# Kernel optimization log

Hardware: AMD Instinct MI355X
Metric: run time of the kernel (lower is better)

The kernel has to match this reference:

```python
import jax, jax.numpy as jnp
import numpy as np


def _lstm_scan(x_tbd, Wih, Whh, bih, bhh):
    """Standard LSTM cell (PyTorch i,f,g,o gate order) scanned over time.
    x_tbd: [T,B,D]; returns hidden states [T,B,H]."""
    H = Whh.shape[1]
    B = x_tbd.shape[1]

    def step(carry, x_t):
        h, c = carry
        gates = x_t @ Wih.T + bih + h @ Whh.T + bhh  # [B,4H]
        i, f, g, o = jnp.split(gates, 4, axis=-1)
        c = jax.nn.sigmoid(f) * c + jax.nn.sigmoid(i) * jnp.tanh(g)
        h = jax.nn.sigmoid(o) * jnp.tanh(c)
        return (h, c), h

    h0 = jnp.zeros((B, H), x_tbd.dtype)
    _, hs = jax.lax.scan(step, (h0, h0), x_tbd)
    return hs


def setup_inputs() -> dict:
    key = jax.random.key(0)
    B, T, D, H = 64, 1024, 512, 256  # output_dim=1024 -> H = output_dim//4 per direction
    ks = jax.random.split(key, 9)
    s = 0.05
    mk = lambda k, shape: jax.random.normal(k, shape, jnp.float32) * s
    return {
        "input": mk(ks[0], (B, T, D)),
        "Wih_f": mk(ks[1], (4 * H, D)), "Whh_f": mk(ks[2], (4 * H, H)),
        "bih_f": mk(ks[3], (4 * H,)),   "bhh_f": mk(ks[4], (4 * H,)),
        "Wih_b": mk(ks[5], (4 * H, D)), "Whh_b": mk(ks[6], (4 * H, H)),
        "bih_b": mk(ks[7], (4 * H,)),   "bhh_b": mk(ks[8], (4 * H,)),
    }


def reference(input, Wih_f, Whh_f, bih_f, bhh_f, Wih_b, Whh_b, bih_b, bhh_b):
    # [B,T,D] -> [T,B,D] for scan over time
    x_tbd = jnp.transpose(input, (1, 0, 2))
    hf = _lstm_scan(x_tbd, Wih_f, Whh_f, bih_f, bhh_f)            # forward in time
    hb = _lstm_scan(x_tbd[::-1], Wih_b, Whh_b, bih_b, bhh_b)[::-1]  # backward, re-aligned
    # output[t] = cat(outputf[t], outputb[T-1-t]) == cat(hf[t], hb_aligned[t])
    out = jnp.concatenate([hf, hb], axis=-1)  # [T,B,2H]
    return jnp.transpose(out, (1, 0, 2))      # [B,T,2H]
```

## Files before the change

### kernel.cpp

```cpp
#include <hip/hip_runtime.h>
#include <hip/hip_bf16.h>

typedef __attribute__((ext_vector_type(8))) short bf8;
typedef __attribute__((ext_vector_type(4))) float f32x4;
typedef __attribute__((ext_vector_type(2))) unsigned int u32x2;

#define T_SEQ 1024

__device__ __forceinline__ float sigm(float x) { return 1.f / (1.f + __expf(-x)); }
__device__ __forceinline__ float tanh_(float x) { return 2.f / (1.f + __expf(-2.f * x)) - 1.f; }

__device__ __forceinline__ short bf16s(float x) {
    union { __hip_bfloat16 h; short s; } u;
    u.h = __float2bfloat16(x);
    return u.s;
}

__device__ __forceinline__ bf8 pack_bf8(const float4 a, const float4 b) {
    bf8 r;
    r[0] = bf16s(a.x); r[1] = bf16s(a.y); r[2] = bf16s(a.z); r[3] = bf16s(a.w);
    r[4] = bf16s(b.x); r[5] = bf16s(b.y); r[6] = bf16s(b.z); r[7] = bf16s(b.w);
    return r;
}

__device__ __forceinline__ void store_sc1_b64(void* p, unsigned int lo, unsigned int hi) {
    u32x2 v; v[0] = lo; v[1] = hi;
    asm volatile("global_store_dwordx2 %0, %1, off sc1" :: "v"(p), "v"(v) : "memory");
}
__device__ __forceinline__ void store_sc1_b32(void* p, unsigned int v) {
    asm volatile("global_store_dword %0, %1, off sc1" :: "v"(p), "v"(v) : "memory");
}
__device__ __forceinline__ unsigned int load_sc1_b32(const void* p) {
    unsigned int v;
    asm volatile("global_load_dword %0, %1, off sc1\n"
                 "s_waitcnt vmcnt(0)"
                 : "=v"(v) : "v"(p) : "memory");
    return v;
}
__device__ __forceinline__ bf8 load_sc1_b128(const void* p) {
    bf8 v;
    asm volatile("global_load_dwordx4 %0, %1, off sc1" : "=v"(v) : "v"(p) : "memory");
    return v;
}

__global__ __launch_bounds__(256) void init_kernel(unsigned int* __restrict__ p, int n)
{
    const int i = blockIdx.x * 256 + threadIdx.x;
    if (i < n) p[i] = 0u;
}

__global__ __launch_bounds__(256) void xproj_kernel(
    const float* __restrict__ X,
    const float* __restrict__ WihF,
    const float* __restrict__ bihF,
    const float* __restrict__ bhhF,
    const float* __restrict__ WihB,
    const float* __restrict__ bihB,
    const float* __restrict__ bhhB,
    __hip_bfloat16* __restrict__ XpF,
    __hip_bfloat16* __restrict__ XpB)
{
    const int dir = blockIdx.z;
    const float* W  = dir ? WihB : WihF;
    const float* bi = dir ? bihB : bihF;
    const float* bh = dir ? bhhB : bhhF;
    __hip_bfloat16* Xp = dir ? XpB : XpF;

    __shared__ __align__(16) short As[128 * 32];
    __shared__ __align__(16) short Bs[128 * 32];

    const int tid  = threadIdx.x;
    const int lane = tid & 63;
    const int w    = tid >> 6;
    const int quad = lane >> 4;
    const int l16  = lane & 15;
    const int wr   = w >> 1, wc = w & 1;

    const int m0 = blockIdx.x * 128;
    const int n0 = blockIdx.y * 128;

    const int srow = tid >> 2;
    const int scg  = tid & 3;

    f32x4 acc[4][4] = {};

    for (int kk = 0; kk < 512; kk += 32) {
        const float* pa0 = X + (size_t)(m0 + srow)      * 512 + kk + scg * 8;
        const float* pa1 = X + (size_t)(m0 + 64 + srow) * 512 + kk + scg * 8;
        const float* pb0 = W + (size_t)(n0 + srow)      * 512 + kk + scg * 8;
        const float* pb1 = W + (size_t)(n0 + 64 + srow) * 512 + kk + scg * 8;
        bf8 a0 = pack_bf8(*(const float4*)pa0, *(const float4*)(pa0 + 4));
        bf8 a1 = pack_bf8(*(const float4*)pa1, *(const float4*)(pa1 + 4));
        bf8 b0 = pack_bf8(*(const float4*)pb0, *(const float4*)(pb0 + 4));
        bf8 b1 = pack_bf8(*(const float4*)pb1, *(const float4*)(pb1 + 4));
        __syncthreads();
        *(bf8*)&As[(srow)      * 32 + scg * 8] = a0;
        *(bf8*)&As[(64 + srow) * 32 + scg * 8] = a1;
        *(bf8*)&Bs[(srow)      * 32 + scg * 8] = b0;
        *(bf8*)&Bs[(64 + srow) * 32 + scg * 8] = b1;
        __syncthreads();

        bf8 af[4], bfr[4];
#pragma unroll
        for (int mt = 0; mt < 4; mt++)
            af[mt] = *(const bf8*)&As[(wr * 64 + mt * 16 + l16) * 32 + quad * 8];
#pragma unroll
        for (int nt = 0; nt < 4; nt++)
            bfr[nt] = *(const bf8*)&Bs[(wc * 64 + nt * 16 + l16) * 32 + quad * 8];
#pragma unroll
        for (int mt = 0; mt < 4; mt++)
#pragma unroll
            for (int nt = 0; nt < 4; nt++)
                acc[mt][nt] = __builtin_amdgcn_mfma_f32_16x16x32_bf16(af[mt], bfr[nt], acc[mt][nt], 0, 0, 0);
    }

#pragma unroll
    for (int nt = 0; nt < 4; nt++) {
        const int n = n0 + wc * 64 + nt * 16 + l16;
        const float bias = bi[n] + bh[n];
#pragma unroll
        for (int mt = 0; mt < 4; mt++) {
#pragma unroll
            for (int r = 0; r < 4; r++) {
                const int m = m0 + wr * 64 + mt * 16 + quad * 4 + r;
                const int b = m >> 10, t = m & 1023;
                Xp[((size_t)t * 64 + b) * 1024 + n] = __float2bfloat16(acc[mt][nt][r] + bias);
            }
        }
    }
}

__global__ __launch_bounds__(256, 1) void lstm_rec_kernel(
    const __hip_bfloat16* __restrict__ XpF,
    const __hip_bfloat16* __restrict__ XpB,
    const float* __restrict__ WhhF,
    const float* __restrict__ WhhB,
    __hip_bfloat16* __restrict__ hexch,
    int* __restrict__ flags,
    float* __restrict__ out)
{
    const int wg  = blockIdx.x;
    const int dir = wg >> 4;
    const int s   = wg & 15;
    const int tid  = threadIdx.x;
    const int lane = tid & 63;
    const int w    = tid >> 6;
    const int quad = lane >> 4;
    const int l16  = lane & 15;

    const __hip_bfloat16* Xp = dir ? XpB : XpF;
    const float* Whh         = dir ? WhhB : WhhF;
    unsigned int* hexchU     = (unsigned int*)hexch;

    __shared__ unsigned int hstage[512];

    bf8 Bf[4][8];
#pragma unroll
    for (int g = 0; g < 4; g++)
#pragma unroll
        for (int k = 0; k < 8; k++) {
            const float* p = Whh + (size_t)(g * 256 + s * 16 + l16) * 256 + k * 32 + quad * 8;
            Bf[g][k] = pack_bf8(*(const float4*)p, *(const float4*)(p + 4));
        }

    float c[4] = {0.f, 0.f, 0.f, 0.f};


    for (int tau = 0; tau < T_SEQ; tau++) {
        const int t = dir ? (T_SEQ - 1 - tau) : tau;

        if (tid < 16) {
            int* f = &flags[(dir * 16 + tid) * 32];
            while ((int)load_sc1_b32(f) < tau) { }
        }
        __syncthreads();

        unsigned short xpu[4][4];
#pragma unroll
        for (int g = 0; g < 4; g++)
#pragma unroll
            for (int r = 0; r < 4; r++) {
                const int b = w * 16 + quad * 4 + r;
                xpu[g][r] = __builtin_nontemporal_load(
                    (const unsigned short*)&Xp[((size_t)t * 64 + b) * 1024 + g * 256 + s * 16 + l16]);
            }

        const __hip_bfloat16* hb = hexch + ((size_t)((tau & 1) * 2 + dir) * 16) * 1024;
        bf8 Af[8];
#pragma unroll
        for (int k = 0; k < 8; k++) {
            const int sA = k * 2 + (quad >> 1);
            Af[k] = load_sc1_b128(hb + (size_t)sA * 1024 + (w * 16 + l16) * 16 + (quad & 1) * 8);
        }
        asm volatile("s_waitcnt vmcnt(0)" ::: "memory");
        __builtin_amdgcn_sched_barrier(0);

        f32x4 acc[4];
        const f32x4 zero = {0.f, 0.f, 0.f, 0.f};
#pragma unroll
        for (int g = 0; g < 4; g++) acc[g] = zero;
#pragma unroll
        for (int k = 0; k < 8; k++)
#pragma unroll
            for (int g = 0; g < 4; g++)
                acc[g] = __builtin_amdgcn_mfma_f32_16x16x32_bf16(Af[k], Bf[g][k], acc[g], 0, 0, 0);

        float hv[4];
#pragma unroll
        for (int r = 0; r < 4; r++) {
            union { unsigned int u; float f; } cv0, cv1, cv2, cv3;
            cv0.u = (unsigned int)xpu[0][r] << 16;
            cv1.u = (unsigned int)xpu[1][r] << 16;
            cv2.u = (unsigned int)xpu[2][r] << 16;
            cv3.u = (unsigned int)xpu[3][r] << 16;
            const float ig = sigm(acc[0][r] + cv0.f);
            const float fg = sigm(acc[1][r] + cv1.f);
            const float gg = tanh_(acc[2][r] + cv2.f);
            const float og = sigm(acc[3][r] + cv3.f);
            c[r] = fg * c[r] + ig * gg;
            hv[r] = og * tanh_(c[r]);
            const int b = w * 16 + quad * 4 + r;
            ((__hip_bfloat16*)hstage)[b * 16 + l16] = __float2bfloat16(hv[r]);
        }
        __syncthreads();

        {
            unsigned int* dst = hexchU + ((size_t)(((tau + 1) & 1) * 2 + dir) * 16 + s) * 512;
            store_sc1_b64(&dst[2 * tid], hstage[2 * tid], hstage[2 * tid + 1]);
        }
        asm volatile("s_waitcnt vmcnt(0)" ::: "memory");
        __syncthreads();
        if (tid == 0)
            store_sc1_b32(&flags[(dir * 16 + s) * 32], (unsigned int)(tau + 1));

#pragma unroll
        for (int r = 0; r < 4; r++) {
            const int b = w * 16 + quad * 4 + r;
            __builtin_nontemporal_store(hv[r], &out[((size_t)b * T_SEQ + t) * 512 + dir * 256 + s * 16 + l16]);
        }
    }
}

extern "C" void kernel_launch(void* const* d_in, const int* in_sizes, int n_in,
                              void* d_out, int out_size, void* d_ws, size_t ws_size,
                              hipStream_t stream)
{
    const float* X    = (const float*)d_in[0];
    const float* WihF = (const float*)d_in[1];
    const float* WhhF = (const float*)d_in[2];
    const float* bihF = (const float*)d_in[3];
    const float* bhhF = (const float*)d_in[4];
    const float* WihB = (const float*)d_in[5];
    const float* WhhB = (const float*)d_in[6];
    const float* bihB = (const float*)d_in[7];
    const float* bhhB = (const float*)d_in[8];
    float* out = (float*)d_out;

    char* ws = (char*)d_ws;
    __hip_bfloat16* XpF   = (__hip_bfloat16*)ws;
    __hip_bfloat16* XpB   = (__hip_bfloat16*)(ws + 134217728);
    __hip_bfloat16* hexch = (__hip_bfloat16*)(ws + 268435456);
    int*            flags = (int*)(ws + 268435456 + 131072);

    const int initN = (131072 + 4096) / 4;
    init_kernel<<<(initN + 255) / 256, 256, 0, stream>>>((unsigned int*)(ws + 268435456), initN);

    dim3 g1(512, 8, 2);
    xproj_kernel<<<g1, 256, 0, stream>>>(X, WihF, bihF, bhhF, WihB, bihB, bhhB, XpF, XpB);
    lstm_rec_kernel<<<32, 256, 0, stream>>>(XpF, XpB, WhhF, WhhB, hexch, flags, out);
}
```

Before: 4.364 ms.

## Replace flag-based handoff with step-tagged hidden-state words in recurrent exchange

```diff
diff --git a/kernel.cpp b/kernel.cpp
--- a/kernel.cpp
+++ b/kernel.cpp
@@ -3,7 +3,7 @@
 
 typedef __attribute__((ext_vector_type(8))) short bf8;
 typedef __attribute__((ext_vector_type(4))) float f32x4;
-typedef __attribute__((ext_vector_type(2))) unsigned int u32x2;
+typedef __attribute__((ext_vector_type(4))) unsigned int u32x4;
 
 #define T_SEQ 1024
 
@@ -23,24 +23,17 @@
     return r;
 }
 
-__device__ __forceinline__ void store_sc1_b64(void* p, unsigned int lo, unsigned int hi) {
-    u32x2 v; v[0] = lo; v[1] = hi;
-    asm volatile("global_store_dwordx2 %0, %1, off sc1" :: "v"(p), "v"(v) : "memory");
-}
 __device__ __forceinline__ void store_sc1_b32(void* p, unsigned int v) {
     asm volatile("global_store_dword %0, %1, off sc1" :: "v"(p), "v"(v) : "memory");
 }
-__device__ __forceinline__ unsigned int load_sc1_b32(const void* p) {
-    unsigned int v;
-    asm volatile("global_load_dword %0, %1, off sc1\n"
-                 "s_waitcnt vmcnt(0)"
-                 : "=v"(v) : "v"(p) : "memory");
-    return v;
-}
-__device__ __forceinline__ bf8 load_sc1_b128(const void* p) {
-    bf8 v;
+__device__ __forceinline__ u32x4 load_sc1_x4(const void* p) {
+    u32x4 v;
     asm volatile("global_load_dwordx4 %0, %1, off sc1" : "=v"(v) : "v"(p) : "memory");
     return v;
+}
+
+__device__ __forceinline__ unsigned short ldnt_u16(const __hip_bfloat16* p) {
+    return __builtin_nontemporal_load((const unsigned short*)p);
 }
 
 __global__ __launch_bounds__(256) void init_kernel(unsigned int* __restrict__ p, int n)
@@ -135,8 +128,7 @@
     const __hip_bfloat16* __restrict__ XpB,
     const float* __restrict__ WhhF,
     const float* __restrict__ WhhB,
-    __hip_bfloat16* __restrict__ hexch,
-    int* __restrict__ flags,
+    unsigned int* __restrict__ ex,
     float* __restrict__ out)
 {
     const int wg  = blockIdx.x;
@@ -150,9 +142,6 @@
 
     const __hip_bfloat16* Xp = dir ? XpB : XpF;
     const float* Whh         = dir ? WhhB : WhhF;
-    unsigned int* hexchU     = (unsigned int*)hexch;
-
-    __shared__ unsigned int hstage[512];
 
     bf8 Bf[4][8];
 #pragma unroll
@@ -165,35 +154,55 @@
 
     float c[4] = {0.f, 0.f, 0.f, 0.f};
 
+    const int crow = quad >> 1;
+    const int coff = (w * 16 + l16) * 16 + (quad & 1) * 8;
+    unsigned int* const exdir = ex + (dir << 14);
 
     for (int tau = 0; tau < T_SEQ; tau++) {
         const int t = dir ? (T_SEQ - 1 - tau) : tau;
 
-        if (tid < 16) {
-            int* f = &flags[(dir * 16 + tid) * 32];
-            while ((int)load_sc1_b32(f) < tau) { }
-        }
-        __syncthreads();
-
         unsigned short xpu[4][4];
 #pragma unroll
         for (int g = 0; g < 4; g++)
 #pragma unroll
             for (int r = 0; r < 4; r++) {
                 const int b = w * 16 + quad * 4 + r;
-                xpu[g][r] = __builtin_nontemporal_load(
-                    (const unsigned short*)&Xp[((size_t)t * 64 + b) * 1024 + g * 256 + s * 16 + l16]);
-            }
-
-        const __hip_bfloat16* hb = hexch + ((size_t)((tau & 1) * 2 + dir) * 16) * 1024;
+                xpu[g][r] = ldnt_u16(&Xp[((size_t)t * 64 + b) * 1024 + g * 256 + s * 16 + l16]);
+            }
+
+        const unsigned int tagw = (unsigned int)tau << 16;
+        unsigned int* const exc = exdir + ((tau & 1) << 15);
+        u32x4 dd[16];
+        int rounds = 0;
+        while (true) {
+#pragma unroll
+            for (int k8 = 0; k8 < 8; k8++) {
+                dd[2 * k8]     = load_sc1_x4(exc + (k8 * 2 + crow) * 1024 + coff);
+                dd[2 * k8 + 1] = load_sc1_x4(exc + (k8 * 2 + crow) * 1024 + coff + 4);
+            }
+            asm volatile("s_waitcnt vmcnt(0)" ::: "memory");
+            __builtin_amdgcn_sched_barrier(0);
+            unsigned int diff = 0;
+#pragma unroll
+            for (int i = 0; i < 16; i++) {
+                diff |= (dd[i][0] ^ tagw) & 0xFFFF0000u;
+                diff |= (dd[i][1] ^ tagw) & 0xFFFF0000u;
+                diff |= (dd[i][2] ^ tagw) & 0xFFFF0000u;
+                diff |= (dd[i][3] ^ tagw) & 0xFFFF0000u;
+            }
+            if (__all(diff == 0)) break;
+            if (++rounds >= 1024) break;
+        }
+
         bf8 Af[8];
 #pragma unroll
-        for (int k = 0; k < 8; k++) {
-            const int sA = k * 2 + (quad >> 1);
-            Af[k] = load_sc1_b128(hb + (size_t)sA * 1024 + (w * 16 + l16) * 16 + (quad & 1) * 8);
-        }
-        asm volatile("s_waitcnt vmcnt(0)" ::: "memory");
-        __builtin_amdgcn_sched_barrier(0);
+        for (int k8 = 0; k8 < 8; k8++) {
+#pragma unroll
+            for (int j = 0; j < 4; j++) {
+                Af[k8][j]     = (short)(dd[2 * k8][j]     & 0xFFFFu);
+                Af[k8][4 + j] = (short)(dd[2 * k8 + 1][j] & 0xFFFFu);
+            }
+        }
 
         f32x4 acc[4];
         const f32x4 zero = {0.f, 0.f, 0.f, 0.f};
@@ -205,6 +214,8 @@
             for (int g = 0; g < 4; g++)
                 acc[g] = __builtin_amdgcn_mfma_f32_16x16x32_bf16(Af[k], Bf[g][k], acc[g], 0, 0, 0);
 
+        const unsigned int pubtag = (unsigned int)(tau + 1) << 16;
+        unsigned int* const dst = exdir + (((tau + 1) & 1) << 15) + (s << 10);
         float hv[4];
 #pragma unroll
         for (int r = 0; r < 4; r++) {
@@ -220,18 +231,9 @@
             c[r] = fg * c[r] + ig * gg;
             hv[r] = og * tanh_(c[r]);
             const int b = w * 16 + quad * 4 + r;
-            ((__hip_bfloat16*)hstage)[b * 16 + l16] = __float2bfloat16(hv[r]);
-        }
-        __syncthreads();
-
-        {
-            unsigned int* dst = hexchU + ((size_t)(((tau + 1) & 1) * 2 + dir) * 16 + s) * 512;
-            store_sc1_b64(&dst[2 * tid], hstage[2 * tid], hstage[2 * tid + 1]);
-        }
-        asm volatile("s_waitcnt vmcnt(0)" ::: "memory");
-        __syncthreads();
-        if (tid == 0)
-            store_sc1_b32(&flags[(dir * 16 + s) * 32], (unsigned int)(tau + 1));
+            store_sc1_b32(&dst[b * 16 + l16],
+                          pubtag | (unsigned int)(unsigned short)bf16s(hv[r]));
+        }
 
 #pragma unroll
         for (int r = 0; r < 4; r++) {
@@ -257,15 +259,14 @@
     float* out = (float*)d_out;
 
     char* ws = (char*)d_ws;
-    __hip_bfloat16* XpF   = (__hip_bfloat16*)ws;
-    __hip_bfloat16* XpB   = (__hip_bfloat16*)(ws + 134217728);
-    __hip_bfloat16* hexch = (__hip_bfloat16*)(ws + 268435456);
-    int*            flags = (int*)(ws + 268435456 + 131072);
-
-    const int initN = (131072 + 4096) / 4;
-    init_kernel<<<(initN + 255) / 256, 256, 0, stream>>>((unsigned int*)(ws + 268435456), initN);
+    __hip_bfloat16* XpF = (__hip_bfloat16*)ws;
+    __hip_bfloat16* XpB = (__hip_bfloat16*)(ws + 134217728);
+    unsigned int*   ex  = (unsigned int*)(ws + 268435456);
+
+    const int initN = 65536;
+    init_kernel<<<initN / 256, 256, 0, stream>>>(ex, initN);
 
     dim3 g1(512, 8, 2);
     xproj_kernel<<<g1, 256, 0, stream>>>(X, WihF, bihF, bhhF, WihB, bihB, bhhB, XpF, XpB);
-    lstm_rec_kernel<<<32, 256, 0, stream>>>(XpF, XpB, WhhF, WhhB, hexch, flags, out);
-}
+    lstm_rec_kernel<<<32, 256, 0, stream>>>(XpF, XpB, WhhF, WhhB, ex, out);
+}
```

Result: slower. 5.335 ms (+22.2%).

## Fuse input projection and recurrence into one kernel with chunked producer-consumer overlap

Applied to the files above, without the earlier changes.

```diff
diff --git a/kernel.cpp b/kernel.cpp
--- a/kernel.cpp
+++ b/kernel.cpp
@@ -29,6 +29,10 @@
 }
 __device__ __forceinline__ void store_sc1_b32(void* p, unsigned int v) {
     asm volatile("global_store_dword %0, %1, off sc1" :: "v"(p), "v"(v) : "memory");
+}
+__device__ __forceinline__ void store_sc1_b16(void* p, unsigned short v) {
+    unsigned int vv = v;
+    asm volatile("global_store_short %0, %1, off sc1" :: "v"(p), "v"(vv) : "memory");
 }
 __device__ __forceinline__ unsigned int load_sc1_b32(const void* p) {
     unsigned int v;
@@ -49,7 +53,7 @@
     if (i < n) p[i] = 0u;
 }
 
-__global__ __launch_bounds__(256) void xproj_kernel(
+__global__ __launch_bounds__(256, 1) void fused_kernel(
     const float* __restrict__ X,
     const float* __restrict__ WihF,
     const float* __restrict__ bihF,
@@ -57,187 +61,201 @@
     const float* __restrict__ WihB,
     const float* __restrict__ bihB,
     const float* __restrict__ bhhB,
+    const float* __restrict__ WhhF,
+    const float* __restrict__ WhhB,
     __hip_bfloat16* __restrict__ XpF,
-    __hip_bfloat16* __restrict__ XpB)
+    __hip_bfloat16* __restrict__ XpB,
+    __hip_bfloat16* __restrict__ hexch,
+    int* __restrict__ flags,
+    int* __restrict__ cnt,
+    float* __restrict__ out)
 {
-    const int dir = blockIdx.z;
-    const float* W  = dir ? WihB : WihF;
-    const float* bi = dir ? bihB : bihF;
-    const float* bh = dir ? bhhB : bhhF;
-    __hip_bfloat16* Xp = dir ? XpB : XpF;
-
-    __shared__ __align__(16) short As[128 * 32];
-    __shared__ __align__(16) short Bs[128 * 32];
-
+    __shared__ __align__(16) unsigned char smem[16384];
     const int tid  = threadIdx.x;
     const int lane = tid & 63;
-    const int w    = tid >> 6;
     const int quad = lane >> 4;
     const int l16  = lane & 15;
-    const int wr   = w >> 1, wc = w & 1;
-
-    const int m0 = blockIdx.x * 128;
-    const int n0 = blockIdx.y * 128;
-
-    const int srow = tid >> 2;
-    const int scg  = tid & 3;
-
-    f32x4 acc[4][4] = {};
-
-    for (int kk = 0; kk < 512; kk += 32) {
-        const float* pa0 = X + (size_t)(m0 + srow)      * 512 + kk + scg * 8;
-        const float* pa1 = X + (size_t)(m0 + 64 + srow) * 512 + kk + scg * 8;
-        const float* pb0 = W + (size_t)(n0 + srow)      * 512 + kk + scg * 8;
-        const float* pb1 = W + (size_t)(n0 + 64 + srow) * 512 + kk + scg * 8;
-        bf8 a0 = pack_bf8(*(const float4*)pa0, *(const float4*)(pa0 + 4));
-        bf8 a1 = pack_bf8(*(const float4*)pa1, *(const float4*)(pa1 + 4));
-        bf8 b0 = pack_bf8(*(const float4*)pb0, *(const float4*)(pb0 + 4));
-        bf8 b1 = pack_bf8(*(const float4*)pb1, *(const float4*)(pb1 + 4));
-        __syncthreads();
-        *(bf8*)&As[(srow)      * 32 + scg * 8] = a0;
-        *(bf8*)&As[(64 + srow) * 32 + scg * 8] = a1;
-        *(bf8*)&Bs[(srow)      * 32 + scg * 8] = b0;
-        *(bf8*)&Bs[(64 + srow) * 32 + scg * 8] = b1;
-        __syncthreads();
-
-        bf8 af[4], bfr[4];
-#pragma unroll
-        for (int mt = 0; mt < 4; mt++)
-            af[mt] = *(const bf8*)&As[(wr * 64 + mt * 16 + l16) * 32 + quad * 8];
-#pragma unroll
-        for (int nt = 0; nt < 4; nt++)
-            bfr[nt] = *(const bf8*)&Bs[(wc * 64 + nt * 16 + l16) * 32 + quad * 8];
-#pragma unroll
-        for (int mt = 0; mt < 4; mt++)
-#pragma unroll
-            for (int nt = 0; nt < 4; nt++)
-                acc[mt][nt] = __builtin_amdgcn_mfma_f32_16x16x32_bf16(af[mt], bfr[nt], acc[mt][nt], 0, 0, 0);
-    }
-
-#pragma unroll
-    for (int nt = 0; nt < 4; nt++) {
-        const int n = n0 + wc * 64 + nt * 16 + l16;
-        const float bias = bi[n] + bh[n];
-#pragma unroll
-        for (int mt = 0; mt < 4; mt++) {
+
+    if (blockIdx.x < 32) {
+        const int wg  = blockIdx.x;
+        const int dir = wg >> 4;
+        const int s   = wg & 15;
+        const int w   = tid >> 6;
+
+        const __hip_bfloat16* Xp = dir ? XpB : XpF;
+        const float* Whh         = dir ? WhhB : WhhF;
+        unsigned int* hexchU     = (unsigned int*)hexch;
+        unsigned int* hstage     = (unsigned int*)smem;
+
+        bf8 Bf[4][8];
+#pragma unroll
+        for (int g = 0; g < 4; g++)
+#pragma unroll
+            for (int k = 0; k < 8; k++) {
+                const float* p = Whh + (size_t)(g * 256 + s * 16 + l16) * 256 + k * 32 + quad * 8;
+                Bf[g][k] = pack_bf8(*(const float4*)p, *(const float4*)(p + 4));
+            }
+
+        float c[4] = {0.f, 0.f, 0.f, 0.f};
+
+        for (int tau = 0; tau < T_SEQ; tau++) {
+            const int t = dir ? (T_SEQ - 1 - tau) : tau;
+
+            if ((tau & 127) == 0) {
+                if (tid == 0) {
+                    const int chunk = dir ? (7 - (tau >> 7)) : (tau >> 7);
+                    const int* cp = &cnt[dir * 8 + chunk];
+                    int guard = 0;
+                    while ((int)load_sc1_b32(cp) < 512 && ++guard < (1 << 20)) { }
+                }
+                __syncthreads();
+            }
+
+            if (tid < 16) {
+                int* f = &flags[(dir * 16 + tid) * 32];
+                while ((int)load_sc1_b32(f) < tau) { }
+            }
+            __syncthreads();
+
+            unsigned short xpu[4][4];
+#pragma unroll
+            for (int g = 0; g < 4; g++)
+#pragma unroll
+                for (int r = 0; r < 4; r++) {
+                    const int b = w * 16 + quad * 4 + r;
+                    xpu[g][r] = __builtin_nontemporal_load(
+                        (const unsigned short*)&Xp[((size_t)t * 64 + b) * 1024 + g * 256 + s * 16 + l16]);
+                }
+
+            const __hip_bfloat16* hb = hexch + ((size_t)((tau & 1) * 2 + dir) * 16) * 1024;
+            bf8 Af[8];
+#pragma unroll
+            for (int k = 0; k < 8; k++) {
+                const int sA = k * 2 + (quad >> 1);
+                Af[k] = load_sc1_b128(hb + (size_t)sA * 1024 + (w * 16 + l16) * 16 + (quad & 1) * 8);
+            }
+            asm volatile("s_waitcnt vmcnt(0)" ::: "memory");
+            __builtin_amdgcn_sched_barrier(0);
+
+            f32x4 acc[4];
+            const f32x4 zero = {0.f, 0.f, 0.f, 0.f};
+#pragma unroll
+            for (int g = 0; g < 4; g++) acc[g] = zero;
+#pragma unroll
+            for (int k = 0; k < 8; k++)
+#pragma unroll
+                for (int g = 0; g < 4; g++)
+                    acc[g] = __builtin_amdgcn_mfma_f32_16x16x32_bf16(Af[k], Bf[g][k], acc[g], 0, 0, 0);
+
+            float hv[4];
 #pragma unroll
             for (int r = 0; r < 4; r++) {
-                const int m = m0 + wr * 64 + mt * 16 + quad * 4 + r;
-                const int b = m >> 10, t = m & 1023;
-                Xp[((size_t)t * 64 + b) * 1024 + n] = __float2bfloat16(acc[mt][nt][r] + bias);
-            }
-        }
-    }
-}
-
-__global__ __launch_bounds__(256, 1) void lstm_rec_kernel(
-    const __hip_bfloat16* __restrict__ XpF,
-    const __hip_bfloat16* __restrict__ XpB,
-    const float* __restrict__ WhhF,
-    const float* __restrict__ WhhB,
-    __hip_bfloat16* __restrict__ hexch,
-    int* __restrict__ flags,
-    float* __restrict__ out)
-{
-    const int wg  = blockIdx.x;
-    const int dir = wg >> 4;
-    const int s   = wg & 15;
-    const int tid  = threadIdx.x;
-    const int lane = tid & 63;
-    const int w    = tid >> 6;
-    const int quad = lane >> 4;
-    const int l16  = lane & 15;
-
-    const __hip_bfloat16* Xp = dir ? XpB : XpF;
-    const float* Whh         = dir ? WhhB : WhhF;
-    unsigned int* hexchU     = (unsigned int*)hexch;
-
-    __shared__ unsigned int hstage[512];
-
-    bf8 Bf[4][8];
-#pragma unroll
-    for (int g = 0; g < 4; g++)
-#pragma unroll
-        for (int k = 0; k < 8; k++) {
-            const float* p = Whh + (size_t)(g * 256 + s * 16 + l16) * 256 + k * 32 + quad * 8;
-            Bf[g][k] = pack_bf8(*(const float4*)p, *(const float4*)(p + 4));
-        }
-
-    float c[4] = {0.f, 0.f, 0.f, 0.f};
-
-
-    for (int tau = 0; tau < T_SEQ; tau++) {
-        const int t = dir ? (T_SEQ - 1 - tau) : tau;
-
-        if (tid < 16) {
-            int* f = &flags[(dir * 16 + tid) * 32];
-            while ((int)load_sc1_b32(f) < tau) { }
-        }
-        __syncthreads();
-
-        unsigned short xpu[4][4];
-#pragma unroll
-        for (int g = 0; g < 4; g++)
+                union { unsigned int u; float f; } cv0, cv1, cv2, cv3;
+                cv0.u = (unsigned int)xpu[0][r] << 16;
+                cv1.u = (unsigned int)xpu[1][r] << 16;
+                cv2.u = (unsigned int)xpu[2][r] << 16;
+                cv3.u = (unsigned int)xpu[3][r] << 16;
+                const float ig = sigm(acc[0][r] + cv0.f);
+                const float fg = sigm(acc[1][r] + cv1.f);
+                const float gg = tanh_(acc[2][r] + cv2.f);
+                const float og = sigm(acc[3][r] + cv3.f);
+                c[r] = fg * c[r] + ig * gg;
+                hv[r] = og * tanh_(c[r]);
+                const int b = w * 16 + quad * 4 + r;
+                ((__hip_bfloat16*)hstage)[b * 16 + l16] = __float2bfloat16(hv[r]);
+            }
+            __syncthreads();
+
+            {
+                unsigned int* dst = hexchU + ((size_t)(((tau + 1) & 1) * 2 + dir) * 16 + s) * 512;
+                store_sc1_b64(&dst[2 * tid], hstage[2 * tid], hstage[2 * tid + 1]);
+            }
+            asm volatile("s_waitcnt vmcnt(0)" ::: "memory");
+            __syncthreads();
+            if (tid == 0)
+                store_sc1_b32(&flags[(dir * 16 + s) * 32], (unsigned int)(tau + 1));
+
 #pragma unroll
             for (int r = 0; r < 4; r++) {
                 const int b = w * 16 + quad * 4 + r;
-                xpu[g][r] = __builtin_nontemporal_load(
-                    (const unsigned short*)&Xp[((size_t)t * 64 + b) * 1024 + g * 256 + s * 16 + l16]);
-            }
-
-        const __hip_bfloat16* hb = hexch + ((size_t)((tau & 1) * 2 + dir) * 16) * 1024;
-        bf8 Af[8];
-#pragma unroll
-        for (int k = 0; k < 8; k++) {
-            const int sA = k * 2 + (quad >> 1);
-            Af[k] = load_sc1_b128(hb + (size_t)sA * 1024 + (w * 16 + l16) * 16 + (quad & 1) * 8);
+                __builtin_nontemporal_store(hv[r], &out[((size_t)b * T_SEQ + t) * 512 + dir * 256 + s * 16 + l16]);
+            }
         }
-        asm volatile("s_waitcnt vmcnt(0)" ::: "memory");
-        __builtin_amdgcn_sched_barrier(0);
-
-        f32x4 acc[4];
-        const f32x4 zero = {0.f, 0.f, 0.f, 0.f};
-#pragma unroll
-        for (int g = 0; g < 4; g++) acc[g] = zero;
-#pragma unroll
-        for (int k = 0; k < 8; k++)
-#pragma unroll
-            for (int g = 0; g < 4; g++)
-                acc[g] = __builtin_amdgcn_mfma_f32_16x16x32_bf16(Af[k], Bf[g][k], acc[g], 0, 0, 0);
-
-        float hv[4];
-#pragma unroll
-        for (int r = 0; r < 4; r++) {
-            union { unsigned int u; float f; } cv0, cv1, cv2, cv3;
-            cv0.u = (unsigned int)xpu[0][r] << 16;
-            cv1.u = (unsigned int)xpu[1][r] << 16;
-            cv2.u = (unsigned int)xpu[2][r] << 16;
-            cv3.u = (unsigned int)xpu[3][r] << 16;
-            const float ig = sigm(acc[0][r] + cv0.f);
-            const float fg = sigm(acc[1][r] + cv1.f);
-            const float gg = tanh_(acc[2][r] + cv2.f);
-            const float og = sigm(acc[3][r] + cv3.f);
-            c[r] = fg * c[r] + ig * gg;
-            hv[r] = og * tanh_(c[r]);
-            const int b = w * 16 + quad * 4 + r;
-            ((__hip_bfloat16*)hstage)[b * 16 + l16] = __float2bfloat16(hv[r]);
+    } else {
+        const int xp4 = blockIdx.x - 32;
+        const int st  = xp4 >> 10;
+        const int r1  = xp4 & 1023;
+        const int dir = r1 >> 9;
+        const int r2  = r1 & 511;
+        const int yb  = r2 >> 6;
+        const int bb  = r2 & 63;
+        const int chunk = dir ? (7 - st) : st;
+        const int m0 = bb * 1024 + chunk * 128;
+        const int n0 = yb * 128;
+
+        const float* W  = dir ? WihB : WihF;
+        const float* bi = dir ? bihB : bihF;
+        const float* bh = dir ? bhhB : bhhF;
+        __hip_bfloat16* Xp = dir ? XpB : XpF;
+
+        short* As = (short*)smem;
+        short* Bs = (short*)(smem + 8192);
+
+        const int w2   = tid >> 6;
+        const int wr   = w2 >> 1, wc = w2 & 1;
+        const int srow = tid >> 2;
+        const int scg  = tid & 3;
+
+        f32x4 acc[4][4] = {};
+
+        for (int kk = 0; kk < 512; kk += 32) {
+            const float* pa0 = X + (size_t)(m0 + srow)      * 512 + kk + scg * 8;
+            const float* pa1 = X + (size_t)(m0 + 64 + srow) * 512 + kk + scg * 8;
+            const float* pb0 = W + (size_t)(n0 + srow)      * 512 + kk + scg * 8;
+            const float* pb1 = W + (size_t)(n0 + 64 + srow) * 512 + kk + scg * 8;
+            bf8 a0 = pack_bf8(*(const float4*)pa0, *(const float4*)(pa0 + 4));
+            bf8 a1 = pack_bf8(*(const float4*)pa1, *(const float4*)(pa1 + 4));
+            bf8 b0 = pack_bf8(*(const float4*)pb0, *(const float4*)(pb0 + 4));
+            bf8 b1 = pack_bf8(*(const float4*)pb1, *(const float4*)(pb1 + 4));
+            __syncthreads();
+            *(bf8*)&As[(srow)      * 32 + scg * 8] = a0;
+            *(bf8*)&As[(64 + srow) * 32 + scg * 8] = a1;
+            *(bf8*)&Bs[(srow)      * 32 + scg * 8] = b0;
+            *(bf8*)&Bs[(64 + srow) * 32 + scg * 8] = b1;
+            __syncthreads();
+
+            bf8 af[4], bfr[4];
+#pragma unroll
+            for (int mt = 0; mt < 4; mt++)
+                af[mt] = *(const bf8*)&As[(wr * 64 + mt * 16 + l16) * 32 + quad * 8];
+#pragma unroll
+            for (int nt = 0; nt < 4; nt++)
+                bfr[nt] = *(const bf8*)&Bs[(wc * 64 + nt * 16 + l16) * 32 + quad * 8];
+#pragma unroll
+            for (int mt = 0; mt < 4; mt++)
+#pragma unroll
+                for (int nt = 0; nt < 4; nt++)
+                    acc[mt][nt] = __builtin_amdgcn_mfma_f32_16x16x32_bf16(af[mt], bfr[nt], acc[mt][nt], 0, 0, 0);
         }
-        __syncthreads();
-
-        {
-            unsigned int* dst = hexchU + ((size_t)(((tau + 1) & 1) * 2 + dir) * 16 + s) * 512;
-            store_sc1_b64(&dst[2 * tid], hstage[2 * tid], hstage[2 * tid + 1]);
+
+#pragma unroll
+        for (int nt = 0; nt < 4; nt++) {
+            const int n = n0 + wc * 64 + nt * 16 + l16;
+            const float bias = bi[n] + bh[n];
+#pragma unroll
+            for (int mt = 0; mt < 4; mt++) {
+#pragma unroll
+                for (int r = 0; r < 4; r++) {
+                    const int m = m0 + wr * 64 + mt * 16 + quad * 4 + r;
+                    const int b = m >> 10, t = m & 1023;
+                    store_sc1_b16(&Xp[((size_t)t * 64 + b) * 1024 + n],
+                                  (unsigned short)bf16s(acc[mt][nt][r] + bias));
+                }
+            }
         }
         asm volatile("s_waitcnt vmcnt(0)" ::: "memory");
         __syncthreads();
-        if (tid == 0)
-            store_sc1_b32(&flags[(dir * 16 + s) * 32], (unsigned int)(tau + 1));
-
-#pragma unroll
-        for (int r = 0; r < 4; r++) {
-            const int b = w * 16 + quad * 4 + r;
-            __builtin_nontemporal_store(hv[r], &out[((size_t)b * T_SEQ + t) * 512 + dir * 256 + s * 16 + l16]);
-        }
+        if (tid == 0) atomicAdd(&cnt[dir * 8 + chunk], 1);
     }
 }
 
@@ -261,11 +279,11 @@
     __hip_bfloat16* XpB   = (__hip_bfloat16*)(ws + 134217728);
     __hip_bfloat16* hexch = (__hip_bfloat16*)(ws + 268435456);
     int*            flags = (int*)(ws + 268435456 + 131072);
-
-    const int initN = (131072 + 4096) / 4;
+    int*            cnt   = (int*)(ws + 268435456 + 131072 + 4096);
+
+    const int initN = (131072 + 4096 + 64) / 4;
     init_kernel<<<(initN + 255) / 256, 256, 0, stream>>>((unsigned int*)(ws + 268435456), initN);
 
-    dim3 g1(512, 8, 2);
-    xproj_kernel<<<g1, 256, 0, stream>>>(X, WihF, bihF, bhhF, WihB, bihB, bhhB, XpF, XpB);
-    lstm_rec_kernel<<<32, 256, 0, stream>>>(XpF, XpB, WhhF, WhhB, hexch, flags, out);
-}
+    fused_kernel<<<8224, 256, 0, stream>>>(X, WihF, bihF, bhhF, WihB, bihB, bhhB,
+                                           WhhF, WhhB, XpF, XpB, hexch, flags, cnt, out);
+}
```

Measured after the change: 4.161 ms. 4.7% less time.
